# Kernel optimization log

Hardware: AMD Instinct MI355X
Metric: run time of the kernel (lower is better)

Reference implementation:

```python
import jax, jax.numpy as jnp
import numpy as np

# ---- static problem dims (mirror the Triton kernel's constexprs) ----
NUM_SEQS = 2
LQ = 1024            # query tokens per sequence (uniform varlen instance)
HIST = 1024          # cached-prefix length per sequence
LK = LQ + HIST       # total kv length per sequence
NUM_HEADS = 32
NUM_KV_HEADS = 8
HEAD_DIM = 128
BLOCK_SIZE = 64
MAX_NUM_BLOCKS = LK // BLOCK_SIZE          # 32 logical blocks per sequence
TOTAL_BLOCKS = NUM_SEQS * MAX_NUM_BLOCKS   # physical blocks in the cache
NEG = -1e10                                # matches kernel's -10000000000.0


def setup_inputs() -> dict:
    key = jax.random.key(0)
    k1, k2, k3, k4 = jax.random.split(key, 4)
    q = jax.random.normal(k1, (NUM_SEQS * LQ, NUM_HEADS, HEAD_DIM), jnp.float32)
    k_cache = jax.random.normal(k2, (TOTAL_BLOCKS, BLOCK_SIZE, NUM_KV_HEADS, HEAD_DIM), jnp.float32)
    v_cache = jax.random.normal(k3, (TOTAL_BLOCKS, BLOCK_SIZE, NUM_KV_HEADS, HEAD_DIM), jnp.float32)
    cu_seqlens_q = (jnp.arange(NUM_SEQS + 1, dtype=jnp.int32) * LQ)
    cu_seqlens_k = (jnp.arange(NUM_SEQS + 1, dtype=jnp.int32) * LK)
    # scattered physical block layout: a random permutation -> irregular gather
    block_tables = jax.random.permutation(k4, TOTAL_BLOCKS).astype(jnp.int32).reshape(NUM_SEQS, MAX_NUM_BLOCKS)
    return dict(q=q, k_cache=k_cache, v_cache=v_cache,
                cu_seqlens_q=cu_seqlens_q, cu_seqlens_k=cu_seqlens_k,
                block_tables=block_tables)


def _paged_prefill_attention(q, k_cache, v_cache, cu_seqlens_q, cu_seqlens_k, block_tables):
    scale = 1.0 / np.sqrt(HEAD_DIM)
    seq_len_q = cu_seqlens_q[1:] - cu_seqlens_q[:-1]            # [S]
    seq_len_k = cu_seqlens_k[1:] - cu_seqlens_k[:-1]            # [S]
    history_len = seq_len_k - seq_len_q                          # [S]

    # uniform varlen instance: flat [total_q, H, D] -> [S, LQ, H, D]
    qr = q.reshape(NUM_SEQS, LQ, NUM_HEADS, HEAD_DIM)
    group = NUM_HEADS // NUM_KV_HEADS
    # [S, LQ, KVH, G, D] so head h maps to kv head h // group (kernel's kv_head_idx)
    q5 = qr.reshape(NUM_SEQS, LQ, NUM_KV_HEADS, group, HEAD_DIM) * scale

    # block-table gather: logical kv layout per sequence
    safe_tables = jnp.maximum(block_tables, 0)
    k = k_cache[safe_tables].reshape(NUM_SEQS, LK, NUM_KV_HEADS, HEAD_DIM)
    v = v_cache[safe_tables].reshape(NUM_SEQS, LK, NUM_KV_HEADS, HEAD_DIM)

    # scores [S, KVH, G, LQ, LK]
    scores = jnp.einsum('sqhgd,skhd->shgqk', q5, k)

    pos_q = jnp.arange(LQ, dtype=jnp.int32)[None, :] + history_len[:, None]   # [S, LQ] absolute positions
    pos_k = jnp.arange(LK, dtype=jnp.int32)                                   # [LK]
    valid_k = (pos_k[None, :] < seq_len_k[:, None]) & \
              jnp.repeat(block_tables >= 0, BLOCK_SIZE, axis=1)               # [S, LK]
    causal = pos_q[:, :, None] >= pos_k[None, None, :]                        # [S, LQ, LK]
    mask = causal & valid_k[:, None, :]
    scores = jnp.where(mask[:, None, None, :, :], scores, NEG)

    p = jax.nn.softmax(scores, axis=-1)  # online-softmax in kernel == exact softmax
    out = jnp.einsum('shgqk,skhd->sqhgd', p, v)
    return out.reshape(NUM_SEQS * LQ, NUM_HEADS, HEAD_DIM)


def reference(q, k_cache, v_cache, cu_seqlens_q, cu_seqlens_k, block_tables):
    return _paged_prefill_attention(q, k_cache, v_cache, cu_seqlens_q, cu_seqlens_k, block_tables)
```

## Files before the change

kernel.cpp:

```cpp
#include <hip/hip_runtime.h>
#include <hip/hip_bf16.h>

#define NS_    2
#define LQ_    1024
#define HIST_  1024
#define LK_    2048
#define NH_    32
#define NKVH_  8
#define HD_    128
#define BS_    64
#define BM_    128
#define MAXB_  32

typedef __attribute__((ext_vector_type(8))) short short8;
typedef __attribute__((ext_vector_type(4))) float f32x4;
typedef __attribute__((ext_vector_type(16))) float f32x16;
typedef __attribute__((ext_vector_type(2))) int int2v;

#define VSTR 72

static __device__ __forceinline__ unsigned short f2bf(float x) {
    __hip_bfloat16 h = __float2bfloat16(x);
    return *(unsigned short*)&h;
}

static __device__ __forceinline__ void cp16(const void* g, void* l) {
    __builtin_amdgcn_global_load_lds(
        (const __attribute__((address_space(1))) void*)g,
        (__attribute__((address_space(3))) void*)l, 16, 0, 0);
}

__global__ __launch_bounds__(256)
void prep_kv(const float* __restrict__ kc, const float* __restrict__ vc,
             const int* __restrict__ bt,
             unsigned short* __restrict__ Kb, unsigned short* __restrict__ Vb)
{
    __shared__ __align__(16) unsigned short Vt[HD_ * VSTR];
    const int tid = threadIdx.x;
    const int gid = blockIdx.x;
    const int seq = gid >> 8;
    const int kvh = (gid >> 5) & 7;
    const int blk = gid & 31;
    const int ph  = bt[seq * MAXB_ + blk];
    const size_t src = ((size_t)ph * BS_ * NKVH_ + kvh) * HD_;
    const int grp = seq * NKVH_ + kvh;
    const int t8 = tid >> 5, q32 = tid & 31;

    float4 kr[8], vr[8];
#pragma unroll
    for (int p = 0; p < 8; ++p)
        kr[p] = *(const float4*)(kc + src + (size_t)(p * 8 + t8) * (NKVH_ * HD_) + q32 * 4);
#pragma unroll
    for (int j = 0; j < 8; ++j)
        vr[j] = *(const float4*)(vc + src + (size_t)(t8 * 8 + j) * (NKVH_ * HD_) + q32 * 4);

#pragma unroll
    for (int p = 0; p < 8; ++p) {
        unsigned short u[4] = {f2bf(kr[p].x), f2bf(kr[p].y), f2bf(kr[p].z), f2bf(kr[p].w)};
        *(uint2*)(Kb + ((size_t)grp * LK_ + blk * BS_ + p * 8 + t8) * HD_ + q32 * 4) = *(const uint2*)u;
    }
#pragma unroll
    for (int w2 = 0; w2 < 4; ++w2) {
        unsigned short row[8];
#pragma unroll
        for (int j = 0; j < 8; ++j) {
            float f = (w2 == 0) ? vr[j].x : (w2 == 1) ? vr[j].y : (w2 == 2) ? vr[j].z : vr[j].w;
            row[j] = f2bf(f);
        }
        *(short8*)&Vt[(q32 * 4 + w2) * VSTR + t8 * 8] = *(const short8*)row;
    }
    __syncthreads();
#pragma unroll
    for (int u = 0; u < 4; ++u) {
        const int c  = tid + 256 * u;
        const int d  = c >> 3, ch = c & 7;
        uint4 x = *(const uint4*)&Vt[d * VSTR + ch * 8];
        *(uint4*)(Vb + ((size_t)grp * HD_ + d) * LK_ + blk * BS_ + ch * 8) = x;
    }
}

template<bool PREP>
__global__ __launch_bounds__(256, 2)
void paged_attn(const float* __restrict__ q,
                const unsigned short* __restrict__ Kb,
                const unsigned short* __restrict__ Vb,
                const float* __restrict__ kc,
                const float* __restrict__ vc,
                const int* __restrict__ bt,
                float* __restrict__ out)
{
    __shared__ __align__(16) unsigned short Ksh[2][BS_ * HD_];
    __shared__ __align__(16) unsigned short Vsh[2][64 * 128];

    const int tid  = threadIdx.x;
    const int w    = tid >> 6;
    const int lane = tid & 63;
    const int m    = lane & 31;
    const int h    = lane >> 5;

    const int gid  = blockIdx.x;
    const int kvh  = gid & 7;
    const int slot = gid >> 3;
    const int seq  = slot >> 5;
    const int sub  = slot & 31;
    const int e    = sub & 1;
    const int t3   = (sub >> 1) & 7;
    const int hp   = sub >> 4;
    const int head = kvh * 4 + hp * 2 + e;
    const int m0   = (e ? (7 - t3) : t3) * BM_;
    const int r0   = m0 + w * 32;
    const int grp  = seq * NKVH_ + kvh;

    const float SC = 0.08838834764831845f * 1.4426950408889634f;
    short8 qf[8];
    {
        const size_t qbase = ((size_t)((seq * LQ_ + r0 + m) * NH_ + head)) * HD_ + h * 8;
#pragma unroll
        for (int c = 0; c < 8; ++c) {
            float4 a = *(const float4*)(q + qbase + c * 16);
            float4 b = *(const float4*)(q + qbase + c * 16 + 4);
            unsigned short u[8] = {f2bf(a.x * SC), f2bf(a.y * SC), f2bf(a.z * SC), f2bf(a.w * SC),
                                   f2bf(b.x * SC), f2bf(b.y * SC), f2bf(b.z * SC), f2bf(b.w * SC)};
            qf[c] = *(const short8*)u;
        }
    }

    f32x16 acc[4];
#pragma unroll
    for (int dt = 0; dt < 4; ++dt)
#pragma unroll
        for (int r = 0; r < 16; ++r) acc[dt][r] = 0.f;
    float lsum = 0.f;

    const int nb = (HIST_ + m0 + BM_ - 1) / BS_ + 1;
    const unsigned short* kSrc = Kb + (size_t)grp * LK_ * HD_;
    const unsigned short* vSrc = Vb + (size_t)grp * HD_ * LK_;

    auto issue = [&](int b, int buf) {
#pragma unroll
        for (int j = 0; j < 4; ++j) {
            const int row = w * 16 + j * 4 + (lane >> 4);
            const int c8  = (lane & 15) ^ (row & 15);
            cp16(kSrc + ((size_t)b * BS_ + row) * HD_ + c8 * 8, &Ksh[buf][(w * 16 + j * 4) * HD_]);
        }
#pragma unroll
        for (int j = 0; j < 4; ++j) {
            const int sr  = w * 16 + j * 4 + (lane >> 4);
            const int cc  = (lane & 15) ^ (sr & 15);
            const int dd  = 2 * sr + (cc >> 3);
            const int cht = cc & 7;
            cp16(vSrc + (size_t)dd * LK_ + b * BS_ + cht * 8, &Vsh[buf][(w * 16 + j * 4) * 128]);
        }
    };

    if constexpr (PREP) issue(0, 0);

    for (int b = 0; b < nb; ++b) {
        const int cur = PREP ? (b & 1) : 0;
        __syncthreads();
        if constexpr (PREP) {
            if (b + 1 < nb) issue(b + 1, 1 ^ cur);
        } else {
            const int ph = bt[seq * MAXB_ + b];
            const size_t src = ((size_t)ph * BS_ * NKVH_ + kvh) * HD_;
#pragma unroll
            for (int j = 0; j < 4; ++j) {
                const int row = w * 16 + j * 4 + (lane >> 4);
                const int c8  = (lane & 15) ^ (row & 15);
                float4 a = *(const float4*)(kc + src + (size_t)row * (NKVH_ * HD_) + c8 * 8);
                float4 b2 = *(const float4*)(kc + src + (size_t)row * (NKVH_ * HD_) + c8 * 8 + 4);
                unsigned short u[8] = {f2bf(a.x), f2bf(a.y), f2bf(a.z), f2bf(a.w),
                                       f2bf(b2.x), f2bf(b2.y), f2bf(b2.z), f2bf(b2.w)};
                *(short8*)&Ksh[0][row * HD_ + (lane & 15) * 8] = *(const short8*)u;
            }
#pragma unroll
            for (int j = 0; j < 4; ++j) {
                const int sr  = w * 16 + j * 4 + (lane >> 4);
                const int cc  = (lane & 15) ^ (sr & 15);
                const int dd  = 2 * sr + (cc >> 3);
                const int cht = cc & 7;
                unsigned short u[8];
#pragma unroll
                for (int i2 = 0; i2 < 8; ++i2)
                    u[i2] = f2bf(vc[src + (size_t)(cht * 8 + i2) * (NKVH_ * HD_) + dd]);
                *(short8*)&Vsh[0][sr * 128 + (lane & 15) * 8] = *(const short8*)u;
            }
            __syncthreads();
        }

        if (64 * b <= HIST_ + r0 + 31) {
            f32x16 s[2];
#pragma unroll
            for (int kt = 0; kt < 2; ++kt)
#pragma unroll
                for (int r = 0; r < 16; ++r) s[kt][r] = 0.f;
            __builtin_amdgcn_s_setprio(1);
#pragma unroll
            for (int c = 0; c < 8; ++c) {
#pragma unroll
                for (int kt = 0; kt < 2; ++kt) {
                    const int row  = kt * 32 + m;
                    const int slt  = (2 * c + h) ^ (row & 15);
                    short8 kf = *(const short8*)&Ksh[cur][row * HD_ + slt * 8];
                    s[kt] = __builtin_amdgcn_mfma_f32_32x32x16_bf16(kf, qf[c], s[kt], 0, 0, 0);
                }
            }
            __builtin_amdgcn_s_setprio(0);

            if (64 * b + 63 > HIST_ + r0) {
                const int thr = HIST_ + r0 + m - 64 * b;
#pragma unroll
                for (int kt = 0; kt < 2; ++kt)
#pragma unroll
                    for (int r = 0; r < 16; ++r) {
                        const int kl = kt * 32 + (r & 3) + 8 * (r >> 2) + 4 * h;
                        if (kl > thr) s[kt][r] = -1e30f;
                    }
            }
            float ls = 0.f;
#pragma unroll
            for (int kt = 0; kt < 2; ++kt)
#pragma unroll
                for (int r = 0; r < 16; ++r) {
                    s[kt][r] = __builtin_amdgcn_exp2f(s[kt][r]);
                    ls += s[kt][r];
                }

            int wlo[8], whi[8];
#pragma unroll
            for (int u = 0; u < 8; ++u) {
                const int kt = u >> 2, rb = (u & 3) * 4;
                int a, bb;
                asm("v_cvt_pk_bf16_f32 %0, %1, %2" : "=v"(a)  : "v"(s[kt][rb]),     "v"(s[kt][rb + 1]));
                asm("v_cvt_pk_bf16_f32 %0, %1, %2" : "=v"(bb) : "v"(s[kt][rb + 2]), "v"(s[kt][rb + 3]));
                wlo[u] = a; whi[u] = bb;
            }
            short8 pf[4];
#pragma unroll
            for (int ks = 0; ks < 4; ++ks) {
                int2v ab = __builtin_amdgcn_permlane32_swap(wlo[2 * ks], wlo[2 * ks + 1], false, false);
                int2v cd = __builtin_amdgcn_permlane32_swap(whi[2 * ks], whi[2 * ks + 1], false, false);
                int w4[4] = { ab[0], cd[0], ab[1], cd[1] };
                pf[ks] = *(const short8*)w4;
            }
            ls += __shfl_xor(ls, 32);
            lsum += ls;

            __builtin_amdgcn_s_setprio(1);
#pragma unroll
            for (int ks = 0; ks < 4; ++ks) {
#pragma unroll
                for (int dt = 0; dt < 4; ++dt) {
                    const int d   = dt * 32 + m;
                    const int sr  = 16 * dt + (m >> 1);
                    const int slt = (((d & 1) << 3) + 2 * ks + h) ^ (sr & 15);
                    short8 vf = *(const short8*)&Vsh[cur][sr * 128 + slt * 8];
                    acc[dt] = __builtin_amdgcn_mfma_f32_32x32x16_bf16(pf[ks], vf, acc[dt], 0, 0, 0);
                }
            }
            __builtin_amdgcn_s_setprio(0);
        }
    }

    {
        const float rl = 1.0f / lsum;
        float rlr[16];
#pragma unroll
        for (int r = 0; r < 16; ++r)
            rlr[r] = __shfl(rl, (r & 3) + 8 * (r >> 2) + 4 * h);
#pragma unroll
        for (int dt = 0; dt < 4; ++dt)
#pragma unroll
            for (int r = 0; r < 16; ++r) {
                const int rloc = (r & 3) + 8 * (r >> 2) + 4 * h;
                out[((size_t)((seq * LQ_ + r0 + rloc) * NH_ + head)) * HD_ + dt * 32 + m] =
                    acc[dt][r] * rlr[r];
            }
    }
}

extern "C" void kernel_launch(void* const* d_in, const int* in_sizes, int n_in,
                              void* d_out, int out_size, void* d_ws, size_t ws_size,
                              hipStream_t stream) {
    const float* q  = (const float*)d_in[0];
    const float* kc = (const float*)d_in[1];
    const float* vc = (const float*)d_in[2];
    const int*   bt = (const int*)d_in[5];
    float*      out = (float*)d_out;
    (void)in_sizes; (void)n_in; (void)out_size;

    const size_t kb_elems = (size_t)NS_ * NKVH_ * LK_ * HD_;
    const size_t need = kb_elems * 2 * sizeof(unsigned short);
    if (ws_size >= need) {
        unsigned short* Kb = (unsigned short*)d_ws;
        unsigned short* Vb = Kb + kb_elems;
        prep_kv<<<512, 256, 0, stream>>>(kc, vc, bt, Kb, Vb);
        paged_attn<true><<<512, 256, 0, stream>>>(q, Kb, Vb, kc, vc, bt, out);
    } else {
        paged_attn<false><<<512, 256, 0, stream>>>(q, nullptr, nullptr, kc, vc, bt, out);
    }
}
```

Before: 170.7 us.

## Split KV block across two wave groups with LDS merge of partial outputs

```diff
diff --git a/kernel.cpp b/kernel.cpp
--- a/kernel.cpp
+++ b/kernel.cpp
@@ -80,7 +80,7 @@
 }
 
 template<bool PREP>
-__global__ __launch_bounds__(256, 2)
+__global__ __launch_bounds__(512, 4)
 void paged_attn(const float* __restrict__ q,
                 const unsigned short* __restrict__ Kb,
                 const unsigned short* __restrict__ Vb,
@@ -89,14 +89,17 @@
                 const int* __restrict__ bt,
                 float* __restrict__ out)
 {
-    __shared__ __align__(16) unsigned short Ksh[2][BS_ * HD_];
-    __shared__ __align__(16) unsigned short Vsh[2][64 * 128];
+    __shared__ __align__(16) unsigned short SH[33280];
+#define KSH(buf) (&SH[(buf) * 8192])
+#define VSH(buf) (&SH[16384 + (buf) * 8192])
 
     const int tid  = threadIdx.x;
-    const int w    = tid >> 6;
+    const int w8   = tid >> 6;
     const int lane = tid & 63;
     const int m    = lane & 31;
     const int h    = lane >> 5;
+    const int rg   = w8 & 3;
+    const int kh   = w8 >> 2;
 
     const int gid  = blockIdx.x;
     const int kvh  = gid & 7;
@@ -108,7 +111,7 @@
     const int hp   = sub >> 4;
     const int head = kvh * 4 + hp * 2 + e;
     const int m0   = (e ? (7 - t3) : t3) * BM_;
-    const int r0   = m0 + w * 32;
+    const int r0   = m0 + rg * 32;
     const int grp  = seq * NKVH_ + kvh;
 
     const float SC = 0.08838834764831845f * 1.4426950408889634f;
@@ -138,18 +141,18 @@
 
     auto issue = [&](int b, int buf) {
 #pragma unroll
-        for (int j = 0; j < 4; ++j) {
-            const int row = w * 16 + j * 4 + (lane >> 4);
+        for (int j = 0; j < 2; ++j) {
+            const int row = w8 * 8 + j * 4 + (lane >> 4);
             const int c8  = (lane & 15) ^ (row & 15);
-            cp16(kSrc + ((size_t)b * BS_ + row) * HD_ + c8 * 8, &Ksh[buf][(w * 16 + j * 4) * HD_]);
-        }
-#pragma unroll
-        for (int j = 0; j < 4; ++j) {
-            const int sr  = w * 16 + j * 4 + (lane >> 4);
+            cp16(kSrc + ((size_t)b * BS_ + row) * HD_ + c8 * 8, &KSH(buf)[(w8 * 8 + j * 4) * HD_]);
+        }
+#pragma unroll
+        for (int j = 0; j < 2; ++j) {
+            const int sr  = w8 * 8 + j * 4 + (lane >> 4);
             const int cc  = (lane & 15) ^ (sr & 15);
             const int dd  = 2 * sr + (cc >> 3);
             const int cht = cc & 7;
-            cp16(vSrc + (size_t)dd * LK_ + b * BS_ + cht * 8, &Vsh[buf][(w * 16 + j * 4) * 128]);
+            cp16(vSrc + (size_t)dd * LK_ + b * BS_ + cht * 8, &VSH(buf)[(w8 * 8 + j * 4) * 128]);
         }
     };
 
@@ -164,18 +167,18 @@
             const int ph = bt[seq * MAXB_ + b];
             const size_t src = ((size_t)ph * BS_ * NKVH_ + kvh) * HD_;
 #pragma unroll
-            for (int j = 0; j < 4; ++j) {
-                const int row = w * 16 + j * 4 + (lane >> 4);
+            for (int j = 0; j < 2; ++j) {
+                const int row = w8 * 8 + j * 4 + (lane >> 4);
                 const int c8  = (lane & 15) ^ (row & 15);
                 float4 a = *(const float4*)(kc + src + (size_t)row * (NKVH_ * HD_) + c8 * 8);
                 float4 b2 = *(const float4*)(kc + src + (size_t)row * (NKVH_ * HD_) + c8 * 8 + 4);
                 unsigned short u[8] = {f2bf(a.x), f2bf(a.y), f2bf(a.z), f2bf(a.w),
                                        f2bf(b2.x), f2bf(b2.y), f2bf(b2.z), f2bf(b2.w)};
-                *(short8*)&Ksh[0][row * HD_ + (lane & 15) * 8] = *(const short8*)u;
-            }
-#pragma unroll
-            for (int j = 0; j < 4; ++j) {
-                const int sr  = w * 16 + j * 4 + (lane >> 4);
+                *(short8*)&KSH(0)[row * HD_ + (lane & 15) * 8] = *(const short8*)u;
+            }
+#pragma unroll
+            for (int j = 0; j < 2; ++j) {
+                const int sr  = w8 * 8 + j * 4 + (lane >> 4);
                 const int cc  = (lane & 15) ^ (sr & 15);
                 const int dd  = 2 * sr + (cc >> 3);
                 const int cht = cc & 7;
@@ -183,61 +186,52 @@
 #pragma unroll
                 for (int i2 = 0; i2 < 8; ++i2)
                     u[i2] = f2bf(vc[src + (size_t)(cht * 8 + i2) * (NKVH_ * HD_) + dd]);
-                *(short8*)&Vsh[0][sr * 128 + (lane & 15) * 8] = *(const short8*)u;
+                *(short8*)&VSH(0)[sr * 128 + (lane & 15) * 8] = *(const short8*)u;
             }
             __syncthreads();
         }
 
-        if (64 * b <= HIST_ + r0 + 31) {
-            f32x16 s[2];
-#pragma unroll
-            for (int kt = 0; kt < 2; ++kt)
-#pragma unroll
-                for (int r = 0; r < 16; ++r) s[kt][r] = 0.f;
+        if (64 * b + kh * 32 <= HIST_ + r0 + 31) {
+            f32x16 s;
+#pragma unroll
+            for (int r = 0; r < 16; ++r) s[r] = 0.f;
+            const int krow = kh * 32 + m;
             __builtin_amdgcn_s_setprio(1);
 #pragma unroll
             for (int c = 0; c < 8; ++c) {
-#pragma unroll
-                for (int kt = 0; kt < 2; ++kt) {
-                    const int row  = kt * 32 + m;
-                    const int slt  = (2 * c + h) ^ (row & 15);
-                    short8 kf = *(const short8*)&Ksh[cur][row * HD_ + slt * 8];
-                    s[kt] = __builtin_amdgcn_mfma_f32_32x32x16_bf16(kf, qf[c], s[kt], 0, 0, 0);
+                const int slt = (2 * c + h) ^ (krow & 15);
+                short8 kf = *(const short8*)&KSH(cur)[krow * HD_ + slt * 8];
+                s = __builtin_amdgcn_mfma_f32_32x32x16_bf16(kf, qf[c], s, 0, 0, 0);
+            }
+            __builtin_amdgcn_s_setprio(0);
+
+            if (64 * b + kh * 32 + 31 > HIST_ + r0) {
+                const int thr = HIST_ + r0 + m - 64 * b - kh * 32;
+#pragma unroll
+                for (int r = 0; r < 16; ++r) {
+                    const int kl = (r & 3) + 8 * (r >> 2) + 4 * h;
+                    if (kl > thr) s[r] = -1e30f;
                 }
             }
-            __builtin_amdgcn_s_setprio(0);
-
-            if (64 * b + 63 > HIST_ + r0) {
-                const int thr = HIST_ + r0 + m - 64 * b;
-#pragma unroll
-                for (int kt = 0; kt < 2; ++kt)
-#pragma unroll
-                    for (int r = 0; r < 16; ++r) {
-                        const int kl = kt * 32 + (r & 3) + 8 * (r >> 2) + 4 * h;
-                        if (kl > thr) s[kt][r] = -1e30f;
-                    }
-            }
             float ls = 0.f;
 #pragma unroll
-            for (int kt = 0; kt < 2; ++kt)
-#pragma unroll
-                for (int r = 0; r < 16; ++r) {
-                    s[kt][r] = __builtin_amdgcn_exp2f(s[kt][r]);
-                    ls += s[kt][r];
-                }
-
-            int wlo[8], whi[8];
-#pragma unroll
-            for (int u = 0; u < 8; ++u) {
-                const int kt = u >> 2, rb = (u & 3) * 4;
+            for (int r = 0; r < 16; ++r) {
+                s[r] = __builtin_amdgcn_exp2f(s[r]);
+                ls += s[r];
+            }
+
+            int wlo[4], whi[4];
+#pragma unroll
+            for (int u = 0; u < 4; ++u) {
+                const int rb = u * 4;
                 int a, bb;
-                asm("v_cvt_pk_bf16_f32 %0, %1, %2" : "=v"(a)  : "v"(s[kt][rb]),     "v"(s[kt][rb + 1]));
-                asm("v_cvt_pk_bf16_f32 %0, %1, %2" : "=v"(bb) : "v"(s[kt][rb + 2]), "v"(s[kt][rb + 3]));
+                asm("v_cvt_pk_bf16_f32 %0, %1, %2" : "=v"(a)  : "v"(s[rb]),     "v"(s[rb + 1]));
+                asm("v_cvt_pk_bf16_f32 %0, %1, %2" : "=v"(bb) : "v"(s[rb + 2]), "v"(s[rb + 3]));
                 wlo[u] = a; whi[u] = bb;
             }
-            short8 pf[4];
-#pragma unroll
-            for (int ks = 0; ks < 4; ++ks) {
+            short8 pf[2];
+#pragma unroll
+            for (int ks = 0; ks < 2; ++ks) {
                 int2v ab = __builtin_amdgcn_permlane32_swap(wlo[2 * ks], wlo[2 * ks + 1], false, false);
                 int2v cd = __builtin_amdgcn_permlane32_swap(whi[2 * ks], whi[2 * ks + 1], false, false);
                 int w4[4] = { ab[0], cd[0], ab[1], cd[1] };
@@ -248,13 +242,13 @@
 
             __builtin_amdgcn_s_setprio(1);
 #pragma unroll
-            for (int ks = 0; ks < 4; ++ks) {
+            for (int ks = 0; ks < 2; ++ks) {
 #pragma unroll
                 for (int dt = 0; dt < 4; ++dt) {
                     const int d   = dt * 32 + m;
                     const int sr  = 16 * dt + (m >> 1);
-                    const int slt = (((d & 1) << 3) + 2 * ks + h) ^ (sr & 15);
-                    short8 vf = *(const short8*)&Vsh[cur][sr * 128 + slt * 8];
+                    const int slt = (((d & 1) << 3) + 4 * kh + 2 * ks + h) ^ (sr & 15);
+                    short8 vf = *(const short8*)&VSH(cur)[sr * 128 + slt * 8];
                     acc[dt] = __builtin_amdgcn_mfma_f32_32x32x16_bf16(pf[ks], vf, acc[dt], 0, 0, 0);
                 }
             }
@@ -262,8 +256,25 @@
         }
     }
 
-    {
-        const float rl = 1.0f / lsum;
+    __syncthreads();
+    float* MG   = (float*)SH;
+    float* base = MG + rg * 4160;
+    if (kh == 1) {
+#pragma unroll
+        for (int dt = 0; dt < 4; ++dt)
+#pragma unroll
+            for (int qq = 0; qq < 4; ++qq) {
+                const int idx = dt * 4 + qq;
+                f32x4 v = (f32x4){acc[dt][qq * 4 + 0], acc[dt][qq * 4 + 1],
+                                  acc[dt][qq * 4 + 2], acc[dt][qq * 4 + 3]};
+                *(f32x4*)&base[lane * 64 + ((idx ^ (lane & 15)) << 2)] = v;
+            }
+        base[4096 + lane] = lsum;
+    }
+    __syncthreads();
+    if (kh == 0) {
+        const float lB = base[4096 + lane];
+        const float rl = 1.0f / (lsum + lB);
         float rlr[16];
 #pragma unroll
         for (int r = 0; r < 16; ++r)
@@ -271,12 +282,20 @@
 #pragma unroll
         for (int dt = 0; dt < 4; ++dt)
 #pragma unroll
-            for (int r = 0; r < 16; ++r) {
-                const int rloc = (r & 3) + 8 * (r >> 2) + 4 * h;
-                out[((size_t)((seq * LQ_ + r0 + rloc) * NH_ + head)) * HD_ + dt * 32 + m] =
-                    acc[dt][r] * rlr[r];
-            }
-    }
+            for (int qq = 0; qq < 4; ++qq) {
+                const int idx = dt * 4 + qq;
+                f32x4 oB = *(const f32x4*)&base[lane * 64 + ((idx ^ (lane & 15)) << 2)];
+#pragma unroll
+                for (int e2 = 0; e2 < 4; ++e2) {
+                    const int r    = qq * 4 + e2;
+                    const int rloc = (r & 3) + 8 * (r >> 2) + 4 * h;
+                    out[((size_t)((seq * LQ_ + r0 + rloc) * NH_ + head)) * HD_ + dt * 32 + m] =
+                        (acc[dt][r] + oB[e2]) * rlr[r];
+                }
+            }
+    }
+#undef KSH
+#undef VSH
 }
 
 extern "C" void kernel_launch(void* const* d_in, const int* in_sizes, int n_in,
@@ -295,8 +314,8 @@
         unsigned short* Kb = (unsigned short*)d_ws;
         unsigned short* Vb = Kb + kb_elems;
         prep_kv<<<512, 256, 0, stream>>>(kc, vc, bt, Kb, Vb);
-        paged_attn<true><<<512, 256, 0, stream>>>(q, Kb, Vb, kc, vc, bt, out);
+        paged_attn<true><<<512, 512, 0, stream>>>(q, Kb, Vb, kc, vc, bt, out);
     } else {
-        paged_attn<false><<<512, 256, 0, stream>>>(q, nullptr, nullptr, kc, vc, bt, out);
-    }
-}
+        paged_attn<false><<<512, 512, 0, stream>>>(q, nullptr, nullptr, kc, vc, bt, out);
+    }
+}
```

Result: slower. 280.5 us (+64.3%).

## Fuse KV prep into attention via cooperative grid sync and defer PV MFMA

Applied to the files above, without the earlier changes.

```diff
diff --git a/kernel.cpp b/kernel.cpp
--- a/kernel.cpp
+++ b/kernel.cpp
@@ -1,5 +1,6 @@
 #include <hip/hip_runtime.h>
 #include <hip/hip_bf16.h>
+#include <hip/hip_cooperative_groups.h>
 
 #define NS_    2
 #define LQ_    1024
@@ -30,67 +31,76 @@
         (__attribute__((address_space(3))) void*)l, 16, 0, 0);
 }
 
+static __device__ __forceinline__ void prep_page(
+    const float* __restrict__ kc, const float* __restrict__ vc,
+    const int* __restrict__ bt,
+    unsigned short* __restrict__ Kb, unsigned short* __restrict__ Vb,
+    unsigned short* Vt,
+    int seq, int kvh, int blk)
+{
+    const int tid = threadIdx.x;
+    const int ph  = bt[seq * MAXB_ + blk];
+    const size_t src = ((size_t)ph * BS_ * NKVH_ + kvh) * HD_;
+    const int grp = seq * NKVH_ + kvh;
+    const int t8 = tid >> 5, q32 = tid & 31;
+
+    float4 kr[8], vr[8];
+#pragma unroll
+    for (int p = 0; p < 8; ++p)
+        kr[p] = *(const float4*)(kc + src + (size_t)(p * 8 + t8) * (NKVH_ * HD_) + q32 * 4);
+#pragma unroll
+    for (int j = 0; j < 8; ++j)
+        vr[j] = *(const float4*)(vc + src + (size_t)(t8 * 8 + j) * (NKVH_ * HD_) + q32 * 4);
+
+#pragma unroll
+    for (int p = 0; p < 8; ++p) {
+        unsigned short u[4] = {f2bf(kr[p].x), f2bf(kr[p].y), f2bf(kr[p].z), f2bf(kr[p].w)};
+        *(uint2*)(Kb + ((size_t)grp * LK_ + blk * BS_ + p * 8 + t8) * HD_ + q32 * 4) = *(const uint2*)u;
+    }
+#pragma unroll
+    for (int w2 = 0; w2 < 4; ++w2) {
+        unsigned short row[8];
+#pragma unroll
+        for (int j = 0; j < 8; ++j) {
+            float f = (w2 == 0) ? vr[j].x : (w2 == 1) ? vr[j].y : (w2 == 2) ? vr[j].z : vr[j].w;
+            row[j] = f2bf(f);
+        }
+        *(short8*)&Vt[(q32 * 4 + w2) * VSTR + t8 * 8] = *(const short8*)row;
+    }
+    __syncthreads();
+#pragma unroll
+    for (int u = 0; u < 4; ++u) {
+        const int c  = tid + 256 * u;
+        const int d  = c >> 3, ch = c & 7;
+        uint4 x = *(const uint4*)&Vt[d * VSTR + ch * 8];
+        *(uint4*)(Vb + ((size_t)grp * HD_ + d) * LK_ + blk * BS_ + ch * 8) = x;
+    }
+    __syncthreads();
+}
+
 __global__ __launch_bounds__(256)
 void prep_kv(const float* __restrict__ kc, const float* __restrict__ vc,
              const int* __restrict__ bt,
              unsigned short* __restrict__ Kb, unsigned short* __restrict__ Vb)
 {
     __shared__ __align__(16) unsigned short Vt[HD_ * VSTR];
-    const int tid = threadIdx.x;
     const int gid = blockIdx.x;
-    const int seq = gid >> 8;
-    const int kvh = (gid >> 5) & 7;
-    const int blk = gid & 31;
-    const int ph  = bt[seq * MAXB_ + blk];
-    const size_t src = ((size_t)ph * BS_ * NKVH_ + kvh) * HD_;
-    const int grp = seq * NKVH_ + kvh;
-    const int t8 = tid >> 5, q32 = tid & 31;
-
-    float4 kr[8], vr[8];
-#pragma unroll
-    for (int p = 0; p < 8; ++p)
-        kr[p] = *(const float4*)(kc + src + (size_t)(p * 8 + t8) * (NKVH_ * HD_) + q32 * 4);
-#pragma unroll
-    for (int j = 0; j < 8; ++j)
-        vr[j] = *(const float4*)(vc + src + (size_t)(t8 * 8 + j) * (NKVH_ * HD_) + q32 * 4);
-
-#pragma unroll
-    for (int p = 0; p < 8; ++p) {
-        unsigned short u[4] = {f2bf(kr[p].x), f2bf(kr[p].y), f2bf(kr[p].z), f2bf(kr[p].w)};
-        *(uint2*)(Kb + ((size_t)grp * LK_ + blk * BS_ + p * 8 + t8) * HD_ + q32 * 4) = *(const uint2*)u;
-    }
-#pragma unroll
-    for (int w2 = 0; w2 < 4; ++w2) {
-        unsigned short row[8];
-#pragma unroll
-        for (int j = 0; j < 8; ++j) {
-            float f = (w2 == 0) ? vr[j].x : (w2 == 1) ? vr[j].y : (w2 == 2) ? vr[j].z : vr[j].w;
-            row[j] = f2bf(f);
-        }
-        *(short8*)&Vt[(q32 * 4 + w2) * VSTR + t8 * 8] = *(const short8*)row;
-    }
-    __syncthreads();
-#pragma unroll
-    for (int u = 0; u < 4; ++u) {
-        const int c  = tid + 256 * u;
-        const int d  = c >> 3, ch = c & 7;
-        uint4 x = *(const uint4*)&Vt[d * VSTR + ch * 8];
-        *(uint4*)(Vb + ((size_t)grp * HD_ + d) * LK_ + blk * BS_ + ch * 8) = x;
-    }
-}
-
-template<bool PREP>
+    prep_page(kc, vc, bt, Kb, Vb, Vt, gid >> 8, (gid >> 5) & 7, gid & 31);
+}
+
+template<int MODE>
 __global__ __launch_bounds__(256, 2)
-void paged_attn(const float* __restrict__ q,
-                const unsigned short* __restrict__ Kb,
-                const unsigned short* __restrict__ Vb,
-                const float* __restrict__ kc,
-                const float* __restrict__ vc,
-                const int* __restrict__ bt,
-                float* __restrict__ out)
+void pattn(const float* __restrict__ q,
+           unsigned short* __restrict__ Kb,
+           unsigned short* __restrict__ Vb,
+           const float* __restrict__ kc,
+           const float* __restrict__ vc,
+           const int* __restrict__ bt,
+           float* __restrict__ out)
 {
-    __shared__ __align__(16) unsigned short Ksh[2][BS_ * HD_];
-    __shared__ __align__(16) unsigned short Vsh[2][64 * 128];
+    __shared__ __align__(16) unsigned short SH[40960];
+#define KSH(buf) (&SH[(buf) * 8192])
+#define VSH(s)   (&SH[16384 + (s) * 8192])
 
     const int tid  = threadIdx.x;
     const int w    = tid >> 6;
@@ -111,6 +121,11 @@
     const int r0   = m0 + w * 32;
     const int grp  = seq * NKVH_ + kvh;
 
+    if constexpr (MODE == 2) {
+        prep_page(kc, vc, bt, Kb, Vb, SH, gid >> 8, kvh, (gid >> 3) & 31);
+        cooperative_groups::this_grid().sync();
+    }
+
     const float SC = 0.08838834764831845f * 1.4426950408889634f;
     short8 qf[8];
     {
@@ -136,12 +151,12 @@
     const unsigned short* kSrc = Kb + (size_t)grp * LK_ * HD_;
     const unsigned short* vSrc = Vb + (size_t)grp * HD_ * LK_;
 
-    auto issue = [&](int b, int buf) {
+    auto issue = [&](int b, int kbuf, int vs) {
 #pragma unroll
         for (int j = 0; j < 4; ++j) {
             const int row = w * 16 + j * 4 + (lane >> 4);
             const int c8  = (lane & 15) ^ (row & 15);
-            cp16(kSrc + ((size_t)b * BS_ + row) * HD_ + c8 * 8, &Ksh[buf][(w * 16 + j * 4) * HD_]);
+            cp16(kSrc + ((size_t)b * BS_ + row) * HD_ + c8 * 8, &KSH(kbuf)[(w * 16 + j * 4) * HD_]);
         }
 #pragma unroll
         for (int j = 0; j < 4; ++j) {
@@ -149,17 +164,41 @@
             const int cc  = (lane & 15) ^ (sr & 15);
             const int dd  = 2 * sr + (cc >> 3);
             const int cht = cc & 7;
-            cp16(vSrc + (size_t)dd * LK_ + b * BS_ + cht * 8, &Vsh[buf][(w * 16 + j * 4) * 128]);
+            cp16(vSrc + (size_t)dd * LK_ + b * BS_ + cht * 8, &VSH(vs)[(w * 16 + j * 4) * 128]);
         }
     };
 
-    if constexpr (PREP) issue(0, 0);
+    auto do_pv = [&](const short8* pfv, int vs) {
+        __builtin_amdgcn_s_setprio(1);
+#pragma unroll
+        for (int ks = 0; ks < 4; ++ks) {
+#pragma unroll
+            for (int dt = 0; dt < 4; ++dt) {
+                const int d   = dt * 32 + m;
+                const int sr  = 16 * dt + (m >> 1);
+                const int slt = (((d & 1) << 3) + 2 * ks + h) ^ (sr & 15);
+                short8 vf = *(const short8*)&VSH(vs)[sr * 128 + slt * 8];
+                acc[dt] = __builtin_amdgcn_mfma_f32_32x32x16_bf16(pfv[ks], vf, acc[dt], 0, 0, 0);
+            }
+        }
+        __builtin_amdgcn_s_setprio(0);
+    };
+
+    if constexpr (MODE >= 1) issue(0, 0, 0);
+
+    int vcur = 0;
+    bool pvalid = false;
+    int pvs = 0;
+    short8 pfp[4];
 
     for (int b = 0; b < nb; ++b) {
-        const int cur = PREP ? (b & 1) : 0;
+        const int cur = (MODE >= 1) ? (b & 1) : 0;
         __syncthreads();
-        if constexpr (PREP) {
-            if (b + 1 < nb) issue(b + 1, 1 ^ cur);
+        if constexpr (MODE >= 1) {
+            if (b + 1 < nb) {
+                int vnx = vcur + 1; if (vnx == 3) vnx = 0;
+                issue(b + 1, 1 ^ cur, vnx);
+            }
         } else {
             const int ph = bt[seq * MAXB_ + b];
             const size_t src = ((size_t)ph * BS_ * NKVH_ + kvh) * HD_;
@@ -171,7 +210,7 @@
                 float4 b2 = *(const float4*)(kc + src + (size_t)row * (NKVH_ * HD_) + c8 * 8 + 4);
                 unsigned short u[8] = {f2bf(a.x), f2bf(a.y), f2bf(a.z), f2bf(a.w),
                                        f2bf(b2.x), f2bf(b2.y), f2bf(b2.z), f2bf(b2.w)};
-                *(short8*)&Ksh[0][row * HD_ + (lane & 15) * 8] = *(const short8*)u;
+                *(short8*)&KSH(0)[row * HD_ + (lane & 15) * 8] = *(const short8*)u;
             }
 #pragma unroll
             for (int j = 0; j < 4; ++j) {
@@ -183,13 +222,14 @@
 #pragma unroll
                 for (int i2 = 0; i2 < 8; ++i2)
                     u[i2] = f2bf(vc[src + (size_t)(cht * 8 + i2) * (NKVH_ * HD_) + dd]);
-                *(short8*)&Vsh[0][sr * 128 + (lane & 15) * 8] = *(const short8*)u;
+                *(short8*)&VSH(0)[sr * 128 + (lane & 15) * 8] = *(const short8*)u;
             }
             __syncthreads();
         }
 
-        if (64 * b <= HIST_ + r0 + 31) {
-            f32x16 s[2];
+        const bool active = (64 * b <= HIST_ + r0 + 31);
+        f32x16 s[2];
+        if (active) {
 #pragma unroll
             for (int kt = 0; kt < 2; ++kt)
 #pragma unroll
@@ -201,12 +241,18 @@
                 for (int kt = 0; kt < 2; ++kt) {
                     const int row  = kt * 32 + m;
                     const int slt  = (2 * c + h) ^ (row & 15);
-                    short8 kf = *(const short8*)&Ksh[cur][row * HD_ + slt * 8];
+                    short8 kf = *(const short8*)&KSH(cur)[row * HD_ + slt * 8];
                     s[kt] = __builtin_amdgcn_mfma_f32_32x32x16_bf16(kf, qf[c], s[kt], 0, 0, 0);
                 }
             }
             __builtin_amdgcn_s_setprio(0);
-
+        }
+
+        if constexpr (MODE >= 1) {
+            if (pvalid) { do_pv(pfp, pvs); pvalid = false; }
+        }
+
+        if (active) {
             if (64 * b + 63 > HIST_ + r0) {
                 const int thr = HIST_ + r0 + m - 64 * b;
 #pragma unroll
@@ -225,7 +271,6 @@
                     s[kt][r] = __builtin_amdgcn_exp2f(s[kt][r]);
                     ls += s[kt][r];
                 }
-
             int wlo[8], whi[8];
 #pragma unroll
             for (int u = 0; u < 8; ++u) {
@@ -235,31 +280,26 @@
                 asm("v_cvt_pk_bf16_f32 %0, %1, %2" : "=v"(bb) : "v"(s[kt][rb + 2]), "v"(s[kt][rb + 3]));
                 wlo[u] = a; whi[u] = bb;
             }
-            short8 pf[4];
 #pragma unroll
             for (int ks = 0; ks < 4; ++ks) {
                 int2v ab = __builtin_amdgcn_permlane32_swap(wlo[2 * ks], wlo[2 * ks + 1], false, false);
                 int2v cd = __builtin_amdgcn_permlane32_swap(whi[2 * ks], whi[2 * ks + 1], false, false);
                 int w4[4] = { ab[0], cd[0], ab[1], cd[1] };
-                pf[ks] = *(const short8*)w4;
+                pfp[ks] = *(const short8*)w4;
             }
             ls += __shfl_xor(ls, 32);
             lsum += ls;
 
-            __builtin_amdgcn_s_setprio(1);
-#pragma unroll
-            for (int ks = 0; ks < 4; ++ks) {
-#pragma unroll
-                for (int dt = 0; dt < 4; ++dt) {
-                    const int d   = dt * 32 + m;
-                    const int sr  = 16 * dt + (m >> 1);
-                    const int slt = (((d & 1) << 3) + 2 * ks + h) ^ (sr & 15);
-                    short8 vf = *(const short8*)&Vsh[cur][sr * 128 + slt * 8];
-                    acc[dt] = __builtin_amdgcn_mfma_f32_32x32x16_bf16(pf[ks], vf, acc[dt], 0, 0, 0);
-                }
-            }
-            __builtin_amdgcn_s_setprio(0);
-        }
+            if constexpr (MODE >= 1) {
+                pvalid = true; pvs = vcur;
+            } else {
+                do_pv(pfp, 0);
+            }
+        }
+        if constexpr (MODE >= 1) { vcur = vcur + 1; if (vcur == 3) vcur = 0; }
+    }
+    if constexpr (MODE >= 1) {
+        if (pvalid) do_pv(pfp, pvs);
     }
 
     {
@@ -277,6 +317,8 @@
                     acc[dt][r] * rlr[r];
             }
     }
+#undef KSH
+#undef VSH
 }
 
 extern "C" void kernel_launch(void* const* d_in, const int* in_sizes, int n_in,
@@ -294,9 +336,28 @@
     if (ws_size >= need) {
         unsigned short* Kb = (unsigned short*)d_ws;
         unsigned short* Vb = Kb + kb_elems;
-        prep_kv<<<512, 256, 0, stream>>>(kc, vc, bt, Kb, Vb);
-        paged_attn<true><<<512, 256, 0, stream>>>(q, Kb, Vb, kc, vc, bt, out);
+
+        static int coopOK = -1;
+        if (coopOK < 0) {
+            void (*fp2)(const float*, unsigned short*, unsigned short*,
+                        const float*, const float*, const int*, float*) = pattn<2>;
+            int nblk = 0;
+            hipError_t err = hipOccupancyMaxActiveBlocksPerMultiprocessor(
+                &nblk, reinterpret_cast<const void*>(fp2), 256, 0);
+            coopOK = (err == hipSuccess && nblk >= 2) ? 1 : 0;
+        }
+        if (coopOK) {
+            void (*fp2)(const float*, unsigned short*, unsigned short*,
+                        const float*, const float*, const int*, float*) = pattn<2>;
+            void* args[] = {(void*)&q, (void*)&Kb, (void*)&Vb,
+                            (void*)&kc, (void*)&vc, (void*)&bt, (void*)&out};
+            hipLaunchCooperativeKernel(reinterpret_cast<const void*>(fp2),
+                                       dim3(512), dim3(256), args, 0, stream);
+        } else {
+            prep_kv<<<512, 256, 0, stream>>>(kc, vc, bt, Kb, Vb);
+            pattn<1><<<512, 256, 0, stream>>>(q, Kb, Vb, kc, vc, bt, out);
+        }
     } else {
-        paged_attn<false><<<512, 256, 0, stream>>>(q, nullptr, nullptr, kc, vc, bt, out);
-    }
-}
+        pattn<0><<<512, 256, 0, stream>>>(q, nullptr, nullptr, kc, vc, bt, out);
+    }
+}
```

New measurement: 170.4 us. About the same (-0.2%).
